# Kernel optimization log

Measured on AMD Instinct MI355X. Metric: run time of the kernel, lower is better.

The kernel has to match this reference:

```python
import jax, jax.numpy as jnp
import numpy as np

D_MODEL = 1024
N_HEADS = 16
D_HEAD = D_MODEL // N_HEADS


def setup_inputs() -> dict:
    key = jax.random.key(0)
    k1, k2, k3 = jax.random.split(key, 3)
    x = jax.random.normal(k1, (2, 2048, D_MODEL), dtype=jnp.float32)
    # torch Linear weights transposed to [in, out] for x @ W
    w_qkv = jax.random.normal(k2, (D_MODEL, 3 * D_MODEL), dtype=jnp.float32) * (D_MODEL ** -0.5)
    w_proj = jax.random.normal(k3, (D_MODEL, D_MODEL), dtype=jnp.float32) * (D_MODEL ** -0.5)
    return {"x": x, "w_qkv": w_qkv, "w_proj": w_proj}


def reference(x, w_qkv, w_proj):
    B, N, D = x.shape
    qkv = x @ w_qkv                              # [B, N, 3D]
    q, k, v = jnp.split(qkv, 3, axis=-1)         # each [B, N, D]

    def split_heads(t):
        return t.reshape(B, N, N_HEADS, D_HEAD).transpose(0, 2, 1, 3)  # [B, H, N, d]

    q, k, v = map(split_heads, (q, k, v))
    scale = 1.0 / jnp.sqrt(jnp.float32(D_HEAD))
    scores = jnp.einsum('bhnd,bhmd->bhnm', q, k) * scale   # [B, H, N, N]
    attn = jax.nn.softmax(scores, axis=-1)
    out = jnp.einsum('bhnm,bhmd->bhnd', attn, v)            # [B, H, N, d]
    out = out.transpose(0, 2, 1, 3).reshape(B, N, D)        # merge heads
    return out @ w_proj + x
```

## Files before the change

kernel.cpp:

```cpp
#include <hip/hip_runtime.h>
#include <hip/hip_bf16.h>
#include <cstdint>
#include <cstddef>

typedef __bf16 bf16;
typedef __attribute__((ext_vector_type(4))) float f32x4;
typedef __attribute__((ext_vector_type(8))) __bf16 bf16x8;
typedef __attribute__((ext_vector_type(4))) __bf16 bf16x4;

#define D_MODEL 1024
#define NHEADS  16
#define DHEAD   64
#define SEQ     2048
#define BATCH   2
#define MROWS   (BATCH*SEQ)
#define BHTOT   (BATCH*NHEADS)

#define QSCALE 0.18033688011112042f
#define DEFER_THR 11.5f

__device__ __forceinline__ void gload16(const bf16* g, bf16* l) {
  __builtin_amdgcn_global_load_lds(
      (const __attribute__((address_space(1))) void*)g,
      (__attribute__((address_space(3))) void*)l, 16, 0, 0);
}

__device__ __forceinline__ f32x4 mfma16(bf16x8 a, bf16x8 b, f32x4 c) {
  return __builtin_amdgcn_mfma_f32_16x16x32_bf16(a, b, c, 0, 0, 0);
}


__global__ void cast_f32_bf16(const float* __restrict__ in, bf16* __restrict__ out, int n4) {
  int i = blockIdx.x * blockDim.x + threadIdx.x;
  if (i >= n4) return;
  float4 v = ((const float4*)in)[i];
  bf16x4 o;
  o[0] = (bf16)v.x; o[1] = (bf16)v.y; o[2] = (bf16)v.z; o[3] = (bf16)v.w;
  ((bf16x4*)out)[i] = o;
}

__global__ void tcast(const float* __restrict__ in, bf16* __restrict__ out, int R, int C) {
  __shared__ float t[32][33];
  int c0 = blockIdx.x * 32, r0 = blockIdx.y * 32;
  int tx = threadIdx.x, ty = threadIdx.y;
  #pragma unroll
  for (int i = 0; i < 4; i++)
    t[ty + i*8][tx] = in[(size_t)(r0 + ty + i*8) * C + c0 + tx];
  __syncthreads();
  #pragma unroll
  for (int i = 0; i < 4; i++)
    out[(size_t)(c0 + ty + i*8) * R + r0 + tx] = (bf16)t[tx][ty + i*8];
}

__global__ void transpose_v(const bf16* __restrict__ v, bf16* __restrict__ vt) {
  __shared__ bf16 t[32][33];
  int bh = blockIdx.z;
  int r0 = blockIdx.x * 32;
  int d0 = blockIdx.y * 32;
  int tx = threadIdx.x, ty = threadIdx.y;
  const bf16* src = v + (size_t)bh * SEQ * DHEAD;
  bf16*       dst = vt + (size_t)bh * DHEAD * SEQ;
  #pragma unroll
  for (int i = 0; i < 4; i++)
    t[ty + i*8][tx] = src[(size_t)(r0 + ty + i*8) * DHEAD + d0 + tx];
  __syncthreads();
  #pragma unroll
  for (int i = 0; i < 4; i++)
    dst[(size_t)(d0 + ty + i*8) * SEQ + r0 + tx] = t[tx][ty + i*8];
}


template <int EPI>
__global__ __launch_bounds__(256) void gemm_bt(
    const bf16* __restrict__ A, const bf16* __restrict__ Bt, int K, int N,
    bf16* __restrict__ qb, bf16* __restrict__ kb, bf16* __restrict__ vb,
    const float* __restrict__ xres, float* __restrict__ outf) {
  __shared__ alignas(16) bf16 As[128 * 32];
  __shared__ alignas(16) bf16 Bs[128 * 32];
  const int tid = threadIdx.x;
  const int wave = tid >> 6, lane = tid & 63;
  const int wr = wave >> 1, wc = wave & 1;
  const int m0 = blockIdx.y * 128, n0 = blockIdx.x * 128;
  const int srow = lane >> 2, scol = (lane & 3) * 8;
  const int lr16 = lane & 15, lg = lane >> 4;

  f32x4 acc[4][4];
  #pragma unroll
  for (int m = 0; m < 4; m++)
    #pragma unroll
    for (int n = 0; n < 4; n++) acc[m][n] = (f32x4)0.0f;

  for (int k0 = 0; k0 < K; k0 += 32) {
    #pragma unroll
    for (int i = 0; i < 2; i++) {
      const int c = i * 4 + wave;
      gload16(A  + (size_t)(m0 + c*16 + srow) * K + k0 + scol, &As[c * 512]);
      gload16(Bt + (size_t)(n0 + c*16 + srow) * K + k0 + scol, &Bs[c * 512]);
    }
    __syncthreads();
    bf16x8 af[4], bfr[4];
    #pragma unroll
    for (int m = 0; m < 4; m++)
      af[m] = *(const bf16x8*)&As[(wr*64 + m*16 + lr16) * 32 + lg * 8];
    #pragma unroll
    for (int n = 0; n < 4; n++)
      bfr[n] = *(const bf16x8*)&Bs[(wc*64 + n*16 + lr16) * 32 + lg * 8];
    #pragma unroll
    for (int m = 0; m < 4; m++)
      #pragma unroll
      for (int n = 0; n < 4; n++)
        acc[m][n] = mfma16(af[m], bfr[n], acc[m][n]);
    __syncthreads();
  }

  #pragma unroll
  for (int n = 0; n < 4; n++) {
    const int colg = n0 + wc*64 + n*16 + lr16;
    if (EPI == 0) {
      const int which = colg >> 10;
      const int win = colg & 1023;
      const int h = win >> 6, d = win & 63;
      bf16* dst = (which == 0) ? qb : (which == 1) ? kb : vb;
      const float sc = (which == 0) ? QSCALE : 1.0f;
      #pragma unroll
      for (int m = 0; m < 4; m++) {
        const int rowg0 = m0 + wr*64 + m*16 + lg*4;
        #pragma unroll
        for (int j = 0; j < 4; j++) {
          const int rowg = rowg0 + j;
          const int b = rowg >> 11, r = rowg & 2047;
          dst[((size_t)((b << 4) + h) * SEQ + r) * DHEAD + d] = (bf16)(acc[m][n][j] * sc);
        }
      }
    } else {
      #pragma unroll
      for (int m = 0; m < 4; m++) {
        const int rowg0 = m0 + wr*64 + m*16 + lg*4;
        #pragma unroll
        for (int j = 0; j < 4; j++) {
          const size_t idx = (size_t)(rowg0 + j) * N + colg;
          outf[idx] = acc[m][n][j] + xres[idx];
        }
      }
    }
  }
}

__global__ __launch_bounds__(512, 6) void attn_kernel(
    const bf16* __restrict__ q, const bf16* __restrict__ k,
    const bf16* __restrict__ vt, bf16* __restrict__ o) {
  __shared__ alignas(16) bf16 Ks[2][64 * 64];
  __shared__ alignas(16) bf16 Vs[2][64 * 64];
  __shared__ alignas(16) bf16 P[8][16 * 72];
  const int tid = threadIdx.x;
  const int wave = tid >> 6, lane = tid & 63;
  const int lr16 = lane & 15, lg = lane >> 4;
  const int bh = blockIdx.y;
  const int b = bh >> 4, h = bh & 15;
  const int qr = blockIdx.x * 128 + wave * 16;
  const bf16* kh = k  + (size_t)bh * SEQ * DHEAD;
  const bf16* vh = vt + (size_t)bh * DHEAD * SEQ;

  const int srow = lane >> 3;
  const int scol = ((lane & 7) ^ srow) * 8;
  const int c = wave;

  const bf16* qrow = q + (size_t)bh * SEQ * DHEAD + (size_t)(qr + lr16) * DHEAD;
  bf16x8 qf[2];
  qf[0] = *(const bf16x8*)&qrow[lg * 8];
  qf[1] = *(const bf16x8*)&qrow[32 + lg * 8];

  float mr = -INFINITY, lsum = 0.0f;
  f32x4 acc[4];
  #pragma unroll
  for (int db = 0; db < 4; db++) acc[db] = (f32x4)0.0f;

  bf16* pw = &P[wave][0];
  const int rsw = (lr16 & 7) << 4;

  gload16(kh + (size_t)(c*8 + srow) * DHEAD + scol, &Ks[0][c * 512]);
  gload16(vh + (size_t)(c*8 + srow) * SEQ + scol,   &Vs[0][c * 512]);
  __syncthreads();

  int buf = 0;
  for (int t = 0; t < SEQ / 64; ++t) {
    if (t + 1 < SEQ / 64) {
      const int kv1 = (t + 1) * 64;
      gload16(kh + (size_t)(kv1 + c*8 + srow) * DHEAD + scol, &Ks[buf ^ 1][c * 512]);
      gload16(vh + (size_t)(c*8 + srow) * SEQ + kv1 + scol,   &Vs[buf ^ 1][c * 512]);
    }

    const char* ksb = (const char*)&Ks[buf][0];
    const char* vsb = (const char*)&Vs[buf][0];

    f32x4 s[4];
    #pragma unroll
    for (int i = 0; i < 4; i++) {
      const int rb = (i * 16 + lr16) * 128;
      bf16x8 kf0 = *(const bf16x8*)(ksb + rb + ((lg * 16) ^ rsw));
      bf16x8 kf1 = *(const bf16x8*)(ksb + rb + ((64 + lg * 16) ^ rsw));
      f32x4 z = (f32x4)0.0f;
      z = mfma16(kf0, qf[0], z);
      z = mfma16(kf1, qf[1], z);
      s[i] = z;
    }

    float a0 = fmaxf(fmaxf(s[0][0], s[0][1]), fmaxf(s[0][2], s[0][3]));
    float a1 = fmaxf(fmaxf(s[1][0], s[1][1]), fmaxf(s[1][2], s[1][3]));
    float a2 = fmaxf(fmaxf(s[2][0], s[2][1]), fmaxf(s[2][2], s[2][3]));
    float a3 = fmaxf(fmaxf(s[3][0], s[3][1]), fmaxf(s[3][2], s[3][3]));
    const float lmax = fmaxf(fmaxf(a0, a1), fmaxf(a2, a3));

    if (!__all(lmax <= mr + DEFER_THR)) {
      float mx = lmax;
      mx = fmaxf(mx, __shfl_xor(mx, 16));
      mx = fmaxf(mx, __shfl_xor(mx, 32));
      const float mnew = fmaxf(mr, mx);
      const float corr = exp2f(mr - mnew);
      lsum *= corr;
      #pragma unroll
      for (int db = 0; db < 4; db++) acc[db] *= corr;
      mr = mnew;
    }

    #pragma unroll
    for (int i = 0; i < 4; i++)
      #pragma unroll
      for (int r = 0; r < 4; r++)
        s[i][r] = exp2f(s[i][r] - mr);
    float rs = 0.0f;
    #pragma unroll
    for (int i = 0; i < 4; i++)
      rs += (s[i][0] + s[i][1]) + (s[i][2] + s[i][3]);
    lsum += rs;

    #pragma unroll
    for (int i = 0; i < 4; i++) {
      bf16x4 pv;
      #pragma unroll
      for (int r = 0; r < 4; r++) pv[r] = (bf16)s[i][r];
      *(bf16x4*)&pw[lr16 * 72 + i * 16 + lg * 4] = pv;
    }
    bf16x8 pf0 = *(const bf16x8*)&pw[lr16 * 72 + lg * 8];
    bf16x8 pf1 = *(const bf16x8*)&pw[lr16 * 72 + 32 + lg * 8];

    #pragma unroll
    for (int db = 0; db < 4; db++) {
      const int rb = (db * 16 + lr16) * 128;
      bf16x8 vf0 = *(const bf16x8*)(vsb + rb + ((lg * 16) ^ rsw));
      bf16x8 vf1 = *(const bf16x8*)(vsb + rb + ((64 + lg * 16) ^ rsw));
      acc[db] = mfma16(vf0, pf0, acc[db]);
      acc[db] = mfma16(vf1, pf1, acc[db]);
    }

    __syncthreads();
    buf ^= 1;
  }

  lsum += __shfl_xor(lsum, 16);
  lsum += __shfl_xor(lsum, 32);
  const float inv = 1.0f / lsum;
  bf16* orow = o + ((size_t)(b * SEQ + qr + lr16)) * D_MODEL + h * 64;
  #pragma unroll
  for (int db = 0; db < 4; db++) {
    bf16x4 ov;
    #pragma unroll
    for (int r = 0; r < 4; r++) ov[r] = (bf16)(acc[db][r] * inv);
    *(bf16x4*)&orow[db * 16 + lg * 4] = ov;
  }
}


extern "C" void kernel_launch(void* const* d_in, const int* in_sizes, int n_in,
                              void* d_out, int out_size, void* d_ws, size_t ws_size,
                              hipStream_t stream) {
  const float* x      = (const float*)d_in[0];
  const float* w_qkv  = (const float*)d_in[1];
  const float* w_proj = (const float*)d_in[2];
  float* outf = (float*)d_out;

  bf16* xb    = (bf16*)d_ws;
  bf16* wqkvT = xb    + (size_t)MROWS * D_MODEL;
  bf16* wpT   = wqkvT + (size_t)3 * D_MODEL * D_MODEL;
  bf16* qb    = wpT   + (size_t)D_MODEL * D_MODEL;
  bf16* kb    = qb    + (size_t)BHTOT * SEQ * DHEAD;
  bf16* vb    = kb    + (size_t)BHTOT * SEQ * DHEAD;
  bf16* vt    = xb;
  bf16* ob    = vb;

  dim3 tb(32, 8);

  cast_f32_bf16<<<(MROWS * D_MODEL / 4 + 255) / 256, 256, 0, stream>>>(
      x, xb, MROWS * D_MODEL / 4);
  tcast<<<dim3(3 * D_MODEL / 32, D_MODEL / 32), tb, 0, stream>>>(
      w_qkv, wqkvT, D_MODEL, 3 * D_MODEL);
  tcast<<<dim3(D_MODEL / 32, D_MODEL / 32), tb, 0, stream>>>(
      w_proj, wpT, D_MODEL, D_MODEL);

  gemm_bt<0><<<dim3(3 * D_MODEL / 128, MROWS / 128), 256, 0, stream>>>(
      xb, wqkvT, D_MODEL, 3 * D_MODEL, qb, kb, vb, nullptr, nullptr);

  transpose_v<<<dim3(SEQ / 32, DHEAD / 32, BHTOT), tb, 0, stream>>>(vb, vt);

  attn_kernel<<<dim3(SEQ / 128, BHTOT), 512, 0, stream>>>(qb, kb, vt, ob);

  gemm_bt<1><<<dim3(D_MODEL / 128, MROWS / 128), 256, 0, stream>>>(
      ob, wpT, D_MODEL, D_MODEL, nullptr, nullptr, nullptr, x, outf);
}
```

Before: 153.6 us.

## Widen GEMM K-tile with swizzled LDS and streamline attention inner loop

The GEMM now stages 64-wide K tiles with an XOR-swizzled LDS layout, which halves the number of barrier pairs and reduces bank conflicts. Its launch bounds add a minimum occupancy of 3 blocks. The attention kernel folds the running-max subtraction into the MFMA accumulator init, uses the raw hardware exp2 instruction, and unrolls the double-buffer loop by two with precomputed pointers. It also raises wave priority around MFMA sections and lowers its occupancy hint from 6 to 4. Risks include register pressure changes and exp2 precision differences.

```diff
diff --git a/kernel.cpp b/kernel.cpp
--- a/kernel.cpp
+++ b/kernel.cpp
@@ -27,6 +27,14 @@
 
 __device__ __forceinline__ f32x4 mfma16(bf16x8 a, bf16x8 b, f32x4 c) {
   return __builtin_amdgcn_mfma_f32_16x16x32_bf16(a, b, c, 0, 0, 0);
+}
+
+__device__ __forceinline__ float fexp2(float x) {
+#if __has_builtin(__builtin_amdgcn_exp2f)
+  return __builtin_amdgcn_exp2f(x);
+#else
+  float r; asm("v_exp_f32 %0, %1" : "=v"(r) : "v"(x)); return r;
+#endif
 }
 
 
@@ -71,18 +79,24 @@
 
 
 template <int EPI>
-__global__ __launch_bounds__(256) void gemm_bt(
+__global__ __launch_bounds__(256, 3) void gemm_bt(
     const bf16* __restrict__ A, const bf16* __restrict__ Bt, int K, int N,
     bf16* __restrict__ qb, bf16* __restrict__ kb, bf16* __restrict__ vb,
     const float* __restrict__ xres, float* __restrict__ outf) {
-  __shared__ alignas(16) bf16 As[128 * 32];
-  __shared__ alignas(16) bf16 Bs[128 * 32];
+  __shared__ alignas(16) bf16 As[128 * 64];
+  __shared__ alignas(16) bf16 Bs[128 * 64];
   const int tid = threadIdx.x;
   const int wave = tid >> 6, lane = tid & 63;
   const int wr = wave >> 1, wc = wave & 1;
   const int m0 = blockIdx.y * 128, n0 = blockIdx.x * 128;
-  const int srow = lane >> 2, scol = (lane & 3) * 8;
+  const int srow = lane >> 3;
+  const int scol = ((lane & 7) ^ srow) * 8;
   const int lr16 = lane & 15, lg = lane >> 4;
+  const int rsw = (lr16 & 7) << 4;
+  const int cA = (lg * 16) ^ rsw;
+  const int cB = (64 + lg * 16) ^ rsw;
+  const char* aP = (const char*)As + (wr*64 + lr16) * 128;
+  const char* bP = (const char*)Bs + (wc*64 + lr16) * 128;
 
   f32x4 acc[4][4];
   #pragma unroll
@@ -90,26 +104,32 @@
     #pragma unroll
     for (int n = 0; n < 4; n++) acc[m][n] = (f32x4)0.0f;
 
-  for (int k0 = 0; k0 < K; k0 += 32) {
-    #pragma unroll
-    for (int i = 0; i < 2; i++) {
-      const int c = i * 4 + wave;
-      gload16(A  + (size_t)(m0 + c*16 + srow) * K + k0 + scol, &As[c * 512]);
-      gload16(Bt + (size_t)(n0 + c*16 + srow) * K + k0 + scol, &Bs[c * 512]);
+  for (int k0 = 0; k0 < K; k0 += 64) {
+    #pragma unroll
+    for (int j = 0; j < 4; j++) {
+      const int c = wave * 4 + j;
+      gload16(A  + (size_t)(m0 + c*8 + srow) * K + k0 + scol, &As[c * 512]);
+      gload16(Bt + (size_t)(n0 + c*8 + srow) * K + k0 + scol, &Bs[c * 512]);
     }
     __syncthreads();
-    bf16x8 af[4], bfr[4];
+    bf16x8 af[4][2], bfr[4][2];
+    #pragma unroll
+    for (int m = 0; m < 4; m++) {
+      af[m][0] = *(const bf16x8*)(aP + m*2048 + cA);
+      af[m][1] = *(const bf16x8*)(aP + m*2048 + cB);
+    }
+    #pragma unroll
+    for (int n = 0; n < 4; n++) {
+      bfr[n][0] = *(const bf16x8*)(bP + n*2048 + cA);
+      bfr[n][1] = *(const bf16x8*)(bP + n*2048 + cB);
+    }
     #pragma unroll
     for (int m = 0; m < 4; m++)
-      af[m] = *(const bf16x8*)&As[(wr*64 + m*16 + lr16) * 32 + lg * 8];
-    #pragma unroll
-    for (int n = 0; n < 4; n++)
-      bfr[n] = *(const bf16x8*)&Bs[(wc*64 + n*16 + lr16) * 32 + lg * 8];
-    #pragma unroll
-    for (int m = 0; m < 4; m++)
-      #pragma unroll
-      for (int n = 0; n < 4; n++)
-        acc[m][n] = mfma16(af[m], bfr[n], acc[m][n]);
+      #pragma unroll
+      for (int n = 0; n < 4; n++) {
+        acc[m][n] = mfma16(af[m][0], bfr[n][0], acc[m][n]);
+        acc[m][n] = mfma16(af[m][1], bfr[n][1], acc[m][n]);
+      }
     __syncthreads();
   }
 
@@ -146,7 +166,7 @@
   }
 }
 
-__global__ __launch_bounds__(512, 6) void attn_kernel(
+__global__ __launch_bounds__(512, 4) void attn_kernel(
     const bf16* __restrict__ q, const bf16* __restrict__ k,
     const bf16* __restrict__ vt, bf16* __restrict__ o) {
   __shared__ alignas(16) bf16 Ks[2][64 * 64];
@@ -163,98 +183,115 @@
 
   const int srow = lane >> 3;
   const int scol = ((lane & 7) ^ srow) * 8;
-  const int c = wave;
+  const bf16* kg = kh + (size_t)(wave*8 + srow) * DHEAD + scol;
+  const bf16* vg = vh + (size_t)(wave*8 + srow) * SEQ + scol;
+  bf16* ldsK0 = &Ks[0][wave * 512];
+  bf16* ldsK1 = &Ks[1][wave * 512];
+  bf16* ldsV0 = &Vs[0][wave * 512];
+  bf16* ldsV1 = &Vs[1][wave * 512];
 
   const bf16* qrow = q + (size_t)bh * SEQ * DHEAD + (size_t)(qr + lr16) * DHEAD;
   bf16x8 qf[2];
   qf[0] = *(const bf16x8*)&qrow[lg * 8];
   qf[1] = *(const bf16x8*)&qrow[32 + lg * 8];
 
-  float mr = -INFINITY, lsum = 0.0f;
+  float mr = 0.0f, lsum = 0.0f;
   f32x4 acc[4];
   #pragma unroll
   for (int db = 0; db < 4; db++) acc[db] = (f32x4)0.0f;
 
-  bf16* pw = &P[wave][0];
   const int rsw = (lr16 & 7) << 4;
-
-  gload16(kh + (size_t)(c*8 + srow) * DHEAD + scol, &Ks[0][c * 512]);
-  gload16(vh + (size_t)(c*8 + srow) * SEQ + scol,   &Vs[0][c * 512]);
-  __syncthreads();
-
-  int buf = 0;
-  for (int t = 0; t < SEQ / 64; ++t) {
-    if (t + 1 < SEQ / 64) {
-      const int kv1 = (t + 1) * 64;
-      gload16(kh + (size_t)(kv1 + c*8 + srow) * DHEAD + scol, &Ks[buf ^ 1][c * 512]);
-      gload16(vh + (size_t)(c*8 + srow) * SEQ + kv1 + scol,   &Vs[buf ^ 1][c * 512]);
-    }
-
-    const char* ksb = (const char*)&Ks[buf][0];
-    const char* vsb = (const char*)&Vs[buf][0];
-
+  const int cA = (lg * 16) ^ rsw;
+  const int cB = (64 + lg * 16) ^ rsw;
+  const char* kr0 = (const char*)&Ks[0][0] + lr16 * 128;
+  const char* kr1 = (const char*)&Ks[1][0] + lr16 * 128;
+  const char* vr0 = (const char*)&Vs[0][0] + lr16 * 128;
+  const char* vr1 = (const char*)&Vs[1][0] + lr16 * 128;
+  bf16* pww = &P[wave][lr16 * 72 + lg * 4];
+  const bf16* pfr = &P[wave][lr16 * 72 + lg * 8];
+
+  auto compute = [&](const char* kr, const char* vr) {
+    const float nmr = -mr;
     f32x4 s[4];
+    __builtin_amdgcn_s_setprio(1);
     #pragma unroll
     for (int i = 0; i < 4; i++) {
-      const int rb = (i * 16 + lr16) * 128;
-      bf16x8 kf0 = *(const bf16x8*)(ksb + rb + ((lg * 16) ^ rsw));
-      bf16x8 kf1 = *(const bf16x8*)(ksb + rb + ((64 + lg * 16) ^ rsw));
-      f32x4 z = (f32x4)0.0f;
+      bf16x8 kf0 = *(const bf16x8*)(kr + i*2048 + cA);
+      bf16x8 kf1 = *(const bf16x8*)(kr + i*2048 + cB);
+      f32x4 z = {nmr, nmr, nmr, nmr};
       z = mfma16(kf0, qf[0], z);
       z = mfma16(kf1, qf[1], z);
       s[i] = z;
     }
-
-    float a0 = fmaxf(fmaxf(s[0][0], s[0][1]), fmaxf(s[0][2], s[0][3]));
-    float a1 = fmaxf(fmaxf(s[1][0], s[1][1]), fmaxf(s[1][2], s[1][3]));
-    float a2 = fmaxf(fmaxf(s[2][0], s[2][1]), fmaxf(s[2][2], s[2][3]));
-    float a3 = fmaxf(fmaxf(s[3][0], s[3][1]), fmaxf(s[3][2], s[3][3]));
-    const float lmax = fmaxf(fmaxf(a0, a1), fmaxf(a2, a3));
-
-    if (!__all(lmax <= mr + DEFER_THR)) {
-      float mx = lmax;
-      mx = fmaxf(mx, __shfl_xor(mx, 16));
+    __builtin_amdgcn_s_setprio(0);
+
+    float u0 = fmaxf(fmaxf(s[0][0], s[0][1]), s[0][2]);
+    float u1 = fmaxf(fmaxf(s[0][3], s[1][0]), s[1][1]);
+    float u2 = fmaxf(fmaxf(s[1][2], s[1][3]), s[2][0]);
+    float u3 = fmaxf(fmaxf(s[2][1], s[2][2]), s[2][3]);
+    float u4 = fmaxf(fmaxf(s[3][0], s[3][1]), s[3][2]);
+    float lmax = fmaxf(fmaxf(fmaxf(u0, u1), fmaxf(u2, u3)), fmaxf(u4, s[3][3]));
+
+    if (!__all(lmax <= DEFER_THR)) {
+      float mx = fmaxf(lmax, __shfl_xor(lmax, 16));
       mx = fmaxf(mx, __shfl_xor(mx, 32));
-      const float mnew = fmaxf(mr, mx);
-      const float corr = exp2f(mr - mnew);
+      mx = fmaxf(mx, 0.0f);
+      const float corr = fexp2(-mx);
       lsum *= corr;
       #pragma unroll
       for (int db = 0; db < 4; db++) acc[db] *= corr;
-      mr = mnew;
+      mr += mx;
+      #pragma unroll
+      for (int i = 0; i < 4; i++)
+        #pragma unroll
+        for (int r = 0; r < 4; r++) s[i][r] -= mx;
     }
 
     #pragma unroll
     for (int i = 0; i < 4; i++)
       #pragma unroll
-      for (int r = 0; r < 4; r++)
-        s[i][r] = exp2f(s[i][r] - mr);
-    float rs = 0.0f;
-    #pragma unroll
-    for (int i = 0; i < 4; i++)
-      rs += (s[i][0] + s[i][1]) + (s[i][2] + s[i][3]);
-    lsum += rs;
+      for (int r = 0; r < 4; r++) s[i][r] = fexp2(s[i][r]);
+    lsum += ((s[0][0] + s[0][1]) + (s[0][2] + s[0][3]))
+          + ((s[1][0] + s[1][1]) + (s[1][2] + s[1][3]))
+          + ((s[2][0] + s[2][1]) + (s[2][2] + s[2][3]))
+          + ((s[3][0] + s[3][1]) + (s[3][2] + s[3][3]));
 
     #pragma unroll
     for (int i = 0; i < 4; i++) {
       bf16x4 pv;
       #pragma unroll
       for (int r = 0; r < 4; r++) pv[r] = (bf16)s[i][r];
-      *(bf16x4*)&pw[lr16 * 72 + i * 16 + lg * 4] = pv;
-    }
-    bf16x8 pf0 = *(const bf16x8*)&pw[lr16 * 72 + lg * 8];
-    bf16x8 pf1 = *(const bf16x8*)&pw[lr16 * 72 + 32 + lg * 8];
-
+      *(bf16x4*)(pww + i * 16) = pv;
+    }
+    bf16x8 pf0 = *(const bf16x8*)pfr;
+    bf16x8 pf1 = *(const bf16x8*)(pfr + 32);
+
+    __builtin_amdgcn_s_setprio(1);
     #pragma unroll
     for (int db = 0; db < 4; db++) {
-      const int rb = (db * 16 + lr16) * 128;
-      bf16x8 vf0 = *(const bf16x8*)(vsb + rb + ((lg * 16) ^ rsw));
-      bf16x8 vf1 = *(const bf16x8*)(vsb + rb + ((64 + lg * 16) ^ rsw));
+      bf16x8 vf0 = *(const bf16x8*)(vr + db*2048 + cA);
+      bf16x8 vf1 = *(const bf16x8*)(vr + db*2048 + cB);
       acc[db] = mfma16(vf0, pf0, acc[db]);
       acc[db] = mfma16(vf1, pf1, acc[db]);
     }
-
+    __builtin_amdgcn_s_setprio(0);
+  };
+
+  gload16(kg, ldsK0); gload16(vg, ldsV0);
+  kg += 64 * DHEAD; vg += 64;
+  __syncthreads();
+
+  for (int t = 0; t < SEQ / 64; t += 2) {
+    gload16(kg, ldsK1); gload16(vg, ldsV1);
+    kg += 64 * DHEAD; vg += 64;
+    compute(kr0, vr0);
     __syncthreads();
-    buf ^= 1;
+    if (t + 2 < SEQ / 64) {
+      gload16(kg, ldsK0); gload16(vg, ldsV0);
+      kg += 64 * DHEAD; vg += 64;
+    }
+    compute(kr1, vr1);
+    __syncthreads();
   }
 
   lsum += __shfl_xor(lsum, 16);
```

After: 131.0 us. 14.7% less time.
